# Performance work log

Measured on AMD Instinct MI355X. Metric: run time of the kernel, lower is better.

The kernel has to match this reference:

```python
import jax, jax.numpy as jnp
import numpy as np

N_NODES = 50000
N_EDGES = 500000
N_GRAPHS = 100
D = 146
N_CLASSES = 10
BN_EPS = 1e-5


def setup_inputs() -> dict:
    key = jax.random.key(0)
    ks = jax.random.split(key, 16)
    nodes_feat = jax.random.normal(ks[0], (N_NODES, D), dtype=jnp.float32)
    src = jax.random.randint(ks[1], (N_EDGES,), 0, N_NODES)
    dst = jax.random.randint(ks[2], (N_EDGES,), 0, N_NODES)
    graph_ids = jnp.sort(jax.random.randint(ks[3], (N_NODES,), 0, N_GRAPHS))
    # snorm_n = 1/sqrt(num_nodes of the graph each node belongs to)
    counts = jax.ops.segment_sum(jnp.ones((N_NODES,), jnp.float32), graph_ids, N_GRAPHS)
    counts = jnp.maximum(counts, 1.0)
    snorm_n = (1.0 / jnp.sqrt(counts))[graph_ids][:, None]
    s = 1.0 / np.sqrt(D)
    W_emb = jax.random.uniform(ks[4], (D, D), jnp.float32, -s, s)
    b_emb = jnp.zeros((D,), jnp.float32)
    # 4 stacked GCN layers (gcn_1, gcn_2, gcn_3, gcn_o)
    Ws = jax.random.uniform(ks[5], (4, D, D), jnp.float32, -s, s)
    bs = jnp.zeros((4, D), jnp.float32)
    gammas = jnp.ones((4, D), jnp.float32)
    betas = jnp.zeros((4, D), jnp.float32)
    # MLPReadout: 146 -> 73 -> 36 -> 10
    h1, h2 = D // 2, D // 4
    W_r0 = jax.random.uniform(ks[6], (D, h1), jnp.float32, -s, s)
    b_r0 = jnp.zeros((h1,), jnp.float32)
    W_r1 = jax.random.uniform(ks[7], (h1, h2), jnp.float32, -1/np.sqrt(h1), 1/np.sqrt(h1))
    b_r1 = jnp.zeros((h2,), jnp.float32)
    W_r2 = jax.random.uniform(ks[8], (h2, N_CLASSES), jnp.float32, -1/np.sqrt(h2), 1/np.sqrt(h2))
    b_r2 = jnp.zeros((N_CLASSES,), jnp.float32)
    return {"nodes_feat": nodes_feat, "snorm_n": snorm_n, "W_emb": W_emb, "b_emb": b_emb,
            "Ws": Ws, "bs": bs, "gammas": gammas, "betas": betas,
            "W_r0": W_r0, "b_r0": b_r0, "W_r1": W_r1, "b_r1": b_r1, "W_r2": W_r2, "b_r2": b_r2,
            "src": src, "dst": dst, "graph_ids": graph_ids}


def _degree_norms(src, dst):
    ones = jnp.ones((src.shape[0],), jnp.float32)
    deg_out = jnp.maximum(jax.ops.segment_sum(ones, src, N_NODES), 1.0)
    deg_in = jnp.maximum(jax.ops.segment_sum(ones, dst, N_NODES), 1.0)
    return jax.lax.rsqrt(deg_out), jax.lax.rsqrt(deg_in)


def _gcn_layer(h, W, b, gamma, beta, snorm_n, src, dst, norm_src, norm_dst):
    # DGL GraphConv(norm='both'): out = D_in^-1/2 * A^T * (D_out^-1/2 * (h W)) + b
    h_in = h
    hW = (h * norm_src[:, None]) @ W                      # [N, D]
    msg = hW[src]                                          # gather [E, D]
    agg = jax.ops.segment_sum(msg, dst, N_NODES)           # scatter-add [N, D]
    h = agg * norm_dst[:, None] + b
    h = h * snorm_n                                        # graph size norm
    # BatchNorm1d, training-mode batch statistics over nodes
    mean = jnp.mean(h, axis=0)
    var = jnp.var(h, axis=0)
    h = (h - mean) * jax.lax.rsqrt(var + BN_EPS) * gamma + beta
    h = jax.nn.relu(h)
    return h_in + h                                        # residual


def _mean_nodes(h, graph_ids):
    counts = jnp.maximum(jax.ops.segment_sum(jnp.ones((N_NODES,), h.dtype), graph_ids, N_GRAPHS), 1.0)
    return jax.ops.segment_sum(h, graph_ids, N_GRAPHS) / counts[:, None]


def reference(nodes_feat, snorm_n, W_emb, b_emb, Ws, bs, gammas, betas,
              W_r0, b_r0, W_r1, b_r1, W_r2, b_r2, src, dst, graph_ids):
    norm_src, norm_dst = _degree_norms(src, dst)
    h = nodes_feat @ W_emb + b_emb
    hg = jnp.zeros((N_GRAPHS, D), h.dtype)
    for i in range(4):
        h = _gcn_layer(h, Ws[i], bs[i], gammas[i], betas[i], snorm_n, src, dst, norm_src, norm_dst)
        hg = hg + _mean_nodes(h, graph_ids)
    # MLPReadout
    z = jax.nn.relu(hg @ W_r0 + b_r0)
    z = jax.nn.relu(z @ W_r1 + b_r1)
    return z @ W_r2 + b_r2
```

## Files before the change

### kernel.cpp

```cpp
#include <hip/hip_runtime.h>
#include <hip/hip_fp16.h>

#define D 146
#define AS 160
#define HWS 80
#define NG 100
#define BN_EPS 1e-5f

typedef _Float16 half8 __attribute__((ext_vector_type(8)));
typedef float f32x4 __attribute__((ext_vector_type(4)));

__global__ void packw_k(const float* __restrict__ Wemb, const float* __restrict__ Ws,
                        __half* __restrict__ Wf)
{
    int idx = blockIdx.x * 256 + threadIdx.x;
    if (idx >= 5 * 5 * 10 * 64 * 8) return;
    int i8 = idx & 7;
    int l  = (idx >> 3) & 63;
    int t  = (idx >> 9) % 10;
    int s  = (idx / (8 * 64 * 10)) % 5;
    int m  = idx / (8 * 64 * 10 * 5);
    int k = s * 32 + ((l >> 4) << 3) + i8;
    int c = t * 16 + (l & 15);
    float v = 0.0f;
    if (k < D && c < D) {
        const float* Wsrc = (m == 0) ? Wemb : (Ws + (size_t)(m - 1) * D * D);
        v = Wsrc[k * D + c];
    }
    Wf[idx] = __float2half(v);
}

__global__ void cvtnodes_k(const float* __restrict__ nodes, __half2* __restrict__ out2, int N)
{
    int idx = blockIdx.x * 256 + threadIdx.x;
    if (idx >= N * HWS) return;
    int r = idx / HWS, j = idx % HWS;
    int c = 2 * j;
    float v0 = (c < D) ? nodes[(size_t)r * D + c] : 0.0f;
    float v1 = (c + 1 < D) ? nodes[(size_t)r * D + c + 1] : 0.0f;
    out2[idx] = __floats2half2_rn(v0, v1);
}

__global__ void deg_k(const int* __restrict__ src, const int* __restrict__ dst,
                      int* __restrict__ co, int* __restrict__ ci, int E)
{
    int e = blockIdx.x * 256 + threadIdx.x;
    if (e >= E) return;
    atomicAdd(&co[src[e]], 1);
    atomicAdd(&ci[dst[e]], 1);
}

__global__ void rsq_k(const int* __restrict__ co, const int* __restrict__ ci,
                      float* __restrict__ ns, float* __restrict__ nd, int N)
{
    int i = blockIdx.x * 256 + threadIdx.x;
    if (i >= N) return;
    ns[i] = rsqrtf(fmaxf((float)co[i], 1.0f));
    nd[i] = rsqrtf(fmaxf((float)ci[i], 1.0f));
}

__global__ __launch_bounds__(256) void pscan1_k(const int* __restrict__ cnt,
                                                int* __restrict__ bsum, int N)
{
    __shared__ int lds[256];
    int t = blockIdx.x * 256 + threadIdx.x;
    lds[threadIdx.x] = (t < N) ? ((cnt[t] + 7) & ~7) : 0;
    __syncthreads();
    for (int s = 128; s > 0; s >>= 1) {
        if (threadIdx.x < s) lds[threadIdx.x] += lds[threadIdx.x + s];
        __syncthreads();
    }
    if (threadIdx.x == 0) bsum[blockIdx.x] = lds[0];
}

__global__ __launch_bounds__(256) void pscan2_k(const int* __restrict__ bsum,
                                                int* __restrict__ boff, int nb)
{
    __shared__ int lds[256];
    int t = threadIdx.x;
    int v = (t < nb) ? bsum[t] : 0;
    lds[t] = v;
    __syncthreads();
    for (int off = 1; off < 256; off <<= 1) {
        int u = (t >= off) ? lds[t - off] : 0;
        __syncthreads();
        lds[t] += u;
        __syncthreads();
    }
    boff[t] = lds[t] - v;
}

__global__ __launch_bounds__(256) void pscan3_k(const int* __restrict__ cnt,
                                                const int* __restrict__ boff,
                                                int* __restrict__ rowptr,
                                                int* __restrict__ cursor, int N)
{
    __shared__ int lds[256];
    int t = blockIdx.x * 256 + threadIdx.x;
    int v = (t < N) ? ((cnt[t] + 7) & ~7) : 0;
    lds[threadIdx.x] = v;
    __syncthreads();
    for (int off = 1; off < 256; off <<= 1) {
        int u = (threadIdx.x >= off) ? lds[threadIdx.x - off] : 0;
        __syncthreads();
        lds[threadIdx.x] += u;
        __syncthreads();
    }
    if (t < N) {
        int r = boff[blockIdx.x] + lds[threadIdx.x] - v;
        rowptr[t] = r;
        cursor[t] = r;
    }
    if (t == N) rowptr[N] = boff[blockIdx.x] + ((N - 1) % 256 < 255 ? 0 : 0);
}

__global__ void rowend_k(const int* __restrict__ cnt, const int* __restrict__ rowptr,
                         int* __restrict__ rowptrN, int N)
{
    if (threadIdx.x == 0 && blockIdx.x == 0)
        rowptrN[0] = rowptr[N - 1] + ((cnt[N - 1] + 7) & ~7);
}

__global__ void padfill_k(const int* __restrict__ cnt, const int* __restrict__ rowptr,
                          int* __restrict__ esrc, int N)
{
    int n = blockIdx.x * 256 + threadIdx.x;
    if (n >= N) return;
    int b = rowptr[n] + cnt[n];
    int ee = rowptr[n] + ((cnt[n] + 7) & ~7);
    for (int i = b; i < ee; ++i) esrc[i] = N;
}

__global__ void csrfill_k(const int* __restrict__ src, const int* __restrict__ dst,
                          int* __restrict__ cursor, int* __restrict__ esrc, int E)
{
    int e = blockIdx.x * 256 + threadIdx.x;
    if (e >= E) return;
    int pos = atomicAdd(&cursor[dst[e]], 1);
    esrc[pos] = src[e];
}

__global__ __launch_bounds__(256) void gemm_mfma(
    const __half* __restrict__ A16, const __half* __restrict__ Wf,
    __half* __restrict__ C16h, __half* __restrict__ H16, int nrows,
    const float* __restrict__ rowscale, const float* __restrict__ bias)
{
    int lane = threadIdx.x & 63, wave = threadIdx.x >> 6;
    int m0 = blockIdx.x * 64 + wave * 16;
    int arow = m0 + (lane & 15);
    if (arow > nrows - 1) arow = nrows - 1;
    int ak = (lane >> 4) * 8;

    f32x4 acc[10] = {};
    const half8* WfV = reinterpret_cast<const half8*>(Wf);
#pragma unroll
    for (int s = 0; s < 5; ++s) {
        half8 a = *reinterpret_cast<const half8*>(&A16[(size_t)arow * AS + s * 32 + ak]);
        const half8* wrow = WfV + (size_t)(s * 10) * 64 + lane;
#pragma unroll
        for (int t = 0; t < 10; ++t) {
            half8 b = wrow[(size_t)t * 64];
            acc[t] = __builtin_amdgcn_mfma_f32_16x16x32_f16(a, b, acc[t], 0, 0, 0);
        }
    }

    int rbase = m0 + (lane >> 4) * 4;
    int ccol = lane & 15;
    if (H16) {
        float rsv[4];
#pragma unroll
        for (int j = 0; j < 4; ++j) {
            int r = rbase + j;
            rsv[j] = (r < nrows) ? rowscale[r] : 0.0f;
        }
#pragma unroll
        for (int t = 0; t < 10; ++t) {
            int c = t * 16 + ccol;
            float bv = (c < D) ? bias[c] : 0.0f;
#pragma unroll
            for (int j = 0; j < 4; ++j) {
                int r = rbase + j;
                if (r >= nrows) continue;
                float v = acc[t][j] + bv;
                H16[(size_t)r * AS + c] = __float2half(v);
                C16h[(size_t)r * AS + c] = __float2half(v * rsv[j]);
            }
        }
    } else {
#pragma unroll
        for (int t = 0; t < 10; ++t) {
            int c = t * 16 + ccol;
            if (c >= D) continue;
#pragma unroll
            for (int j = 0; j < 4; ++j) {
                int r = rbase + j;
                if (r >= nrows) continue;
                C16h[(size_t)r * AS + c] = __float2half(acc[t][j]);
            }
        }
    }
}

__global__ __launch_bounds__(256) void agg_k(
    const __half2* __restrict__ hW2, const int* __restrict__ esrc,
    const int* __restrict__ rowptr,
    const float* __restrict__ nd, const float* __restrict__ sn,
    const float* __restrict__ bias,
    __half2* __restrict__ hpre2, float* __restrict__ stats, int N)
{
    __shared__ float rs[4][D];
    __shared__ float rq[4][D];
    int lane = threadIdx.x & 63, wave = threadIdx.x >> 6;
    int per = (N + gridDim.x - 1) / gridDim.x;
    int n0 = blockIdx.x * per;
    int n1 = min(N, n0 + per);
    int wper = (per + 3) >> 2;
    int w0 = min(n1, n0 + wave * wper);
    int w1 = min(n1, w0 + wper);

    bool v1 = lane < 9;
    int j0 = lane, j1 = 64 + lane;
    int c0 = 2 * lane, c1 = 128 + 2 * lane;
    int c1m = v1 ? c1 : 0;
    float b00 = bias[c0], b01 = bias[c0 + 1];
    float b10 = bias[c1m], b11 = bias[c1m + 1];
    float s00 = 0, s01 = 0, s10 = 0, s11 = 0, q00 = 0, q01 = 0, q10 = 0, q11 = 0;

    int e = (w0 < w1) ? rowptr[w0] : 0;
    for (int n = w0; n < w1; ++n) {
        int ee = rowptr[n + 1];
        float a00 = 0, a01 = 0, a10 = 0, a11 = 0;
        for (; e < ee; e += 8) {
            int4 i0 = *reinterpret_cast<const int4*>(&esrc[e]);
            int4 i1 = *reinterpret_cast<const int4*>(&esrc[e + 4]);
            const __half2* p0 = hW2 + (size_t)i0.x * HWS;
            const __half2* p1 = hW2 + (size_t)i0.y * HWS;
            const __half2* p2 = hW2 + (size_t)i0.z * HWS;
            const __half2* p3 = hW2 + (size_t)i0.w * HWS;
            const __half2* p4 = hW2 + (size_t)i1.x * HWS;
            const __half2* p5 = hW2 + (size_t)i1.y * HWS;
            const __half2* p6 = hW2 + (size_t)i1.z * HWS;
            const __half2* p7 = hW2 + (size_t)i1.w * HWS;
            float2 f0 = __half22float2(p0[j0]);
            float2 f1 = __half22float2(p1[j0]);
            float2 f2 = __half22float2(p2[j0]);
            float2 f3 = __half22float2(p3[j0]);
            float2 f4 = __half22float2(p4[j0]);
            float2 f5 = __half22float2(p5[j0]);
            float2 f6 = __half22float2(p6[j0]);
            float2 f7 = __half22float2(p7[j0]);
            a00 += ((f0.x + f1.x) + (f2.x + f3.x)) + ((f4.x + f5.x) + (f6.x + f7.x));
            a01 += ((f0.y + f1.y) + (f2.y + f3.y)) + ((f4.y + f5.y) + (f6.y + f7.y));
            if (v1) {
                float2 g0 = __half22float2(p0[j1]);
                float2 g1 = __half22float2(p1[j1]);
                float2 g2 = __half22float2(p2[j1]);
                float2 g3 = __half22float2(p3[j1]);
                float2 g4 = __half22float2(p4[j1]);
                float2 g5 = __half22float2(p5[j1]);
                float2 g6 = __half22float2(p6[j1]);
                float2 g7 = __half22float2(p7[j1]);
                a10 += ((g0.x + g1.x) + (g2.x + g3.x)) + ((g4.x + g5.x) + (g6.x + g7.x));
                a11 += ((g0.y + g1.y) + (g2.y + g3.y)) + ((g4.y + g5.y) + (g6.y + g7.y));
            }
        }
        float ndv = nd[n], snv = sn[n];
        float h00 = (a00 * ndv + b00) * snv;
        float h01 = (a01 * ndv + b01) * snv;
        hpre2[(size_t)n * (D / 2) + j0] = __floats2half2_rn(h00, h01);
        s00 += h00; q00 = fmaf(h00, h00, q00);
        s01 += h01; q01 = fmaf(h01, h01, q01);
        if (v1) {
            float h10 = (a10 * ndv + b10) * snv;
            float h11 = (a11 * ndv + b11) * snv;
            hpre2[(size_t)n * (D / 2) + j1] = __floats2half2_rn(h10, h11);
            s10 += h10; q10 = fmaf(h10, h10, q10);
            s11 += h11; q11 = fmaf(h11, h11, q11);
        }
    }
    rs[wave][c0] = s00; rs[wave][c0 + 1] = s01;
    rq[wave][c0] = q00; rq[wave][c0 + 1] = q01;
    if (v1) {
        rs[wave][c1] = s10; rs[wave][c1 + 1] = s11;
        rq[wave][c1] = q10; rq[wave][c1 + 1] = q11;
    }
    __syncthreads();
    for (int cc = threadIdx.x; cc < D; cc += 256) {
        atomicAdd(&stats[cc], rs[0][cc] + rs[1][cc] + rs[2][cc] + rs[3][cc]);
        atomicAdd(&stats[D + cc], rq[0][cc] + rq[1][cc] + rq[2][cc] + rq[3][cc]);
    }
}

__global__ __launch_bounds__(256) void p2hg_k(
    __half2* __restrict__ h2, const __half2* __restrict__ hpre2,
    const float* __restrict__ stats, const float* __restrict__ gamma,
    const float* __restrict__ beta, const float* __restrict__ sn,
    const float* __restrict__ nsrc, const int* __restrict__ gid,
    __half2* __restrict__ hs2, float* __restrict__ hg, int N)
{
    int lane = threadIdx.x & 63, wave = threadIdx.x >> 6;
    int per = (N + gridDim.x - 1) / gridDim.x;
    int n0 = blockIdx.x * per;
    int n1 = min(N, n0 + per);
    int wper = (per + 3) >> 2;
    int w0 = min(n1, n0 + wave * wper);
    int w1 = min(n1, w0 + wper);
    if (w0 >= w1) return;

    bool v1 = lane < 9;
    bool wr = (hs2 != nullptr);
    int j0 = lane, j1 = 64 + lane;
    int c0 = 2 * lane, c1 = 128 + 2 * lane;
    int c1m = v1 ? c1 : 0;
    float inv = 1.0f / (float)N;
    float m00 = stats[c0] * inv,     m01 = stats[c0 + 1] * inv;
    float m10 = stats[c1m] * inv,    m11 = stats[c1m + 1] * inv;
    float v00 = fmaxf(stats[D + c0] * inv - m00 * m00, 0.0f);
    float v01 = fmaxf(stats[D + c0 + 1] * inv - m01 * m01, 0.0f);
    float v10 = fmaxf(stats[D + c1m] * inv - m10 * m10, 0.0f);
    float v11 = fmaxf(stats[D + c1m + 1] * inv - m11 * m11, 0.0f);
    float r00 = rsqrtf(v00 + BN_EPS), r01 = rsqrtf(v01 + BN_EPS);
    float r10 = rsqrtf(v10 + BN_EPS), r11 = rsqrtf(v11 + BN_EPS);
    float g00 = gamma[c0], g01 = gamma[c0 + 1], t00 = beta[c0], t01 = beta[c0 + 1];
    float g10 = gamma[c1m], g11 = gamma[c1m + 1], t10 = beta[c1m], t11 = beta[c1m + 1];

    int g = gid[w0];
    float a00 = 0, a01 = 0, a10 = 0, a11 = 0;
    for (int n = w0; n < w1; ++n) {
        int gr = gid[n];
        if (gr != g) {
            atomicAdd(&hg[(size_t)g * D + c0], a00);
            atomicAdd(&hg[(size_t)g * D + c0 + 1], a01);
            if (v1) {
                atomicAdd(&hg[(size_t)g * D + c1], a10);
                atomicAdd(&hg[(size_t)g * D + c1 + 1], a11);
            }
            a00 = a01 = a10 = a11 = 0;
            g = gr;
        }
        float ns = nsrc[n];
        float w2 = sn[n]; w2 *= w2;
        float2 hv = __half22float2(h2[(size_t)n * HWS + j0]);
        float2 p0 = __half22float2(hpre2[(size_t)n * (D / 2) + j0]);
        float x0 = hv.x + fmaxf((p0.x - m00) * r00 * g00 + t00, 0.0f);
        float x1 = hv.y + fmaxf((p0.y - m01) * r01 * g01 + t01, 0.0f);
        if (wr) {
            h2[(size_t)n * HWS + j0] = __floats2half2_rn(x0, x1);
            hs2[(size_t)n * HWS + j0] = __floats2half2_rn(x0 * ns, x1 * ns);
        }
        a00 = fmaf(x0, w2, a00);
        a01 = fmaf(x1, w2, a01);
        if (v1) {
            float2 hv1 = __half22float2(h2[(size_t)n * HWS + j1]);
            float2 p1 = __half22float2(hpre2[(size_t)n * (D / 2) + j1]);
            float x2 = hv1.x + fmaxf((p1.x - m10) * r10 * g10 + t10, 0.0f);
            float x3 = hv1.y + fmaxf((p1.y - m11) * r11 * g11 + t11, 0.0f);
            if (wr) {
                h2[(size_t)n * HWS + j1] = __floats2half2_rn(x2, x3);
                hs2[(size_t)n * HWS + j1] = __floats2half2_rn(x2 * ns, x3 * ns);
            }
            a10 = fmaf(x2, w2, a10);
            a11 = fmaf(x3, w2, a11);
        }
    }
    atomicAdd(&hg[(size_t)g * D + c0], a00);
    atomicAdd(&hg[(size_t)g * D + c0 + 1], a01);
    if (v1) {
        atomicAdd(&hg[(size_t)g * D + c1], a10);
        atomicAdd(&hg[(size_t)g * D + c1 + 1], a11);
    }
}

__global__ __launch_bounds__(128) void readout_k(
    const float* __restrict__ hg,
    const float* __restrict__ W0, const float* __restrict__ b0,
    const float* __restrict__ W1, const float* __restrict__ b1,
    const float* __restrict__ W2, const float* __restrict__ b2,
    float* __restrict__ out)
{
    __shared__ float hl[D];
    __shared__ float z1[73];
    __shared__ float z2[36];
    int g = blockIdx.x;
    int t = threadIdx.x;
    for (int i = t; i < D; i += 128) hl[i] = hg[(size_t)g * D + i];
    __syncthreads();
    if (t < 73) {
        float s = b0[t];
        for (int k = 0; k < D; ++k) s = fmaf(hl[k], W0[k * 73 + t], s);
        z1[t] = fmaxf(s, 0.0f);
    }
    __syncthreads();
    if (t < 36) {
        float s = b1[t];
        for (int k = 0; k < 73; ++k) s = fmaf(z1[k], W1[k * 36 + t], s);
        z2[t] = fmaxf(s, 0.0f);
    }
    __syncthreads();
    if (t < 10) {
        float s = b2[t];
        for (int k = 0; k < 36; ++k) s = fmaf(z2[k], W2[k * 10 + t], s);
        out[g * 10 + t] = s;
    }
}

extern "C" void kernel_launch(void* const* d_in, const int* in_sizes, int n_in,
                              void* d_out, int out_size, void* d_ws, size_t ws_size,
                              hipStream_t stream)
{
    const float* nodes  = (const float*)d_in[0];
    const float* snorm  = (const float*)d_in[1];
    const float* Wemb   = (const float*)d_in[2];
    const float* bemb   = (const float*)d_in[3];
    const float* Ws     = (const float*)d_in[4];
    const float* bs     = (const float*)d_in[5];
    const float* gammas = (const float*)d_in[6];
    const float* betas  = (const float*)d_in[7];
    const float* Wr0    = (const float*)d_in[8];
    const float* br0    = (const float*)d_in[9];
    const float* Wr1    = (const float*)d_in[10];
    const float* br1    = (const float*)d_in[11];
    const float* Wr2    = (const float*)d_in[12];
    const float* br2    = (const float*)d_in[13];
    const int*   src    = (const int*)d_in[14];
    const int*   dst    = (const int*)d_in[15];
    const int*   gid    = (const int*)d_in[16];

    int N = in_sizes[0] / D;
    int E = in_sizes[14];
    int nb = (N + 255) / 256;
    const int NWF = 5 * 5 * 10 * 64 * 8;
    int Ecap = E + 8 * ((N + 7) & ~7);

    float* ws = (float*)d_ws;
    size_t off = 0;
    float* nsrc  = ws + off; off += N;
    float* ndst  = ws + off; off += N;
    float* stats = ws + off; off += 4 * 4 * D;
    float* hg    = ws + off; off += (size_t)NG * D;
    int* cnt_out = (int*)(ws + off); off += N;
    int* cnt_in  = (int*)(ws + off); off += N;
    int* rowptr  = (int*)(ws + off); off += N + 4;
    int* cursor  = (int*)(ws + off); off += N;
    int* esrc    = (int*)(ws + off); off += Ecap;
    int* bsum    = (int*)(ws + off); off += 256;
    int* boff    = (int*)(ws + off); off += 256;
    off = (off + 3) & ~(size_t)3;
    __half* Wf      = (__half*)(ws + off); off += NWF / 2;
    __half* h16     = (__half*)(ws + off); off += (size_t)N * AS / 2;
    __half* hs16    = (__half*)(ws + off); off += (size_t)N * AS / 2;
    __half* nodes16 = (__half*)(ws + off);
    __half* hW16    = (__half*)(ws + off); off += (size_t)(N + 1) * AS / 2;

    __half* hpre16  = (__half*)(ws + off); off += (size_t)N * D / 2;

    hipMemsetAsync(cnt_out, 0, 2 * (size_t)N * sizeof(int), stream);
    hipMemsetAsync(stats, 0, (16 * D + (size_t)NG * D) * sizeof(float), stream);
    hipMemsetAsync(hW16 + (size_t)N * AS, 0, AS * sizeof(__half), stream);
    packw_k<<<(NWF + 255) / 256, 256, 0, stream>>>(Wemb, Ws, Wf);
    cvtnodes_k<<<(N * HWS + 255) / 256, 256, 0, stream>>>(nodes, (__half2*)nodes16, N);
    deg_k<<<(E + 255) / 256, 256, 0, stream>>>(src, dst, cnt_out, cnt_in, E);
    rsq_k<<<(N + 255) / 256, 256, 0, stream>>>(cnt_out, cnt_in, nsrc, ndst, N);
    pscan1_k<<<nb, 256, 0, stream>>>(cnt_in, bsum, N);
    pscan2_k<<<1, 256, 0, stream>>>(bsum, boff, nb);
    pscan3_k<<<nb, 256, 0, stream>>>(cnt_in, boff, rowptr, cursor, N);
    rowend_k<<<1, 64, 0, stream>>>(cnt_in, rowptr, rowptr + N, N);
    padfill_k<<<nb, 256, 0, stream>>>(cnt_in, rowptr, esrc, N);
    csrfill_k<<<(E + 255) / 256, 256, 0, stream>>>(src, dst, cursor, esrc, E);

    int gblk = (N + 63) / 64;
    gemm_mfma<<<gblk, 256, 0, stream>>>(nodes16, Wf, hs16, h16, N, nsrc, bemb);

    for (int l = 0; l < 4; ++l) {
        float* st = stats + (size_t)l * 4 * D;
        gemm_mfma<<<gblk, 256, 0, stream>>>(hs16, Wf + (size_t)(l + 1) * (NWF / 5),
                                            hW16, nullptr, N, nullptr, nullptr);
        agg_k<<<1024, 256, 0, stream>>>((const __half2*)hW16, esrc, rowptr, ndst, snorm,
                                        bs + (size_t)l * D, (__half2*)hpre16, st, N);
        p2hg_k<<<2048, 256, 0, stream>>>((__half2*)h16, (const __half2*)hpre16, st,
                                         gammas + (size_t)l * D, betas + (size_t)l * D,
                                         snorm, nsrc, gid,
                                         (l == 3) ? nullptr : (__half2*)hs16, hg, N);
    }

    readout_k<<<NG, 128, 0, stream>>>(hg, Wr0, br0, Wr1, br1, Wr2, br2, (float*)d_out);
}
```

Baseline: 566.7 us.

## Balance aggregation work by edge count and compute two row tiles per GEMM wave

A new partition kernel binary-searches the padded CSR row pointer so that each aggregation wave gets a roughly equal share of edges instead of an equal count of nodes. The MFMA GEMM now has each wave compute two 16-row tiles that share the same weight fragments, which halves weight loads per output row. The cost is more accumulator registers per wave and half as many GEMM blocks, which could reduce occupancy and how evenly the blocks spread across compute units. A dead store of rowptr[N] in the scan kernel is also removed.

New measurement: 556.5 us. No clear change (-1.8%).

```diff
diff --git a/kernel.cpp b/kernel.cpp
--- a/kernel.cpp
+++ b/kernel.cpp
@@ -111,7 +111,6 @@
         rowptr[t] = r;
         cursor[t] = r;
     }
-    if (t == N) rowptr[N] = boff[blockIdx.x] + ((N - 1) % 256 < 255 ? 0 : 0);
 }
 
 __global__ void rowend_k(const int* __restrict__ cnt, const int* __restrict__ rowptr,
@@ -140,62 +139,120 @@
     esrc[pos] = src[e];
 }
 
+__global__ void part_k(const int* __restrict__ rowptr, int* __restrict__ wstart,
+                       int N, int NW)
+{
+    int w = blockIdx.x * 256 + threadIdx.x;
+    if (w > NW) return;
+    if (w == NW) { wstart[NW] = N; return; }
+    if (w == 0) { wstart[0] = 0; return; }
+    long long Epad = rowptr[N];
+    long long target = Epad * w / NW;
+    int lo = 0, hi = N;
+    while (lo < hi) {
+        int mid = (lo + hi) >> 1;
+        if ((long long)rowptr[mid] <= target) lo = mid + 1; else hi = mid;
+    }
+    wstart[w] = lo - 1;
+}
+
 __global__ __launch_bounds__(256) void gemm_mfma(
     const __half* __restrict__ A16, const __half* __restrict__ Wf,
     __half* __restrict__ C16h, __half* __restrict__ H16, int nrows,
     const float* __restrict__ rowscale, const float* __restrict__ bias)
 {
     int lane = threadIdx.x & 63, wave = threadIdx.x >> 6;
-    int m0 = blockIdx.x * 64 + wave * 16;
-    int arow = m0 + (lane & 15);
-    if (arow > nrows - 1) arow = nrows - 1;
+    int m0 = blockIdx.x * 128 + wave * 32;
+    int ar0 = min(m0 + (lane & 15), nrows - 1);
+    int ar1 = min(m0 + 16 + (lane & 15), nrows - 1);
     int ak = (lane >> 4) * 8;
 
-    f32x4 acc[10] = {};
+    f32x4 acc0[10] = {};
+    f32x4 acc1[10] = {};
     const half8* WfV = reinterpret_cast<const half8*>(Wf);
 #pragma unroll
     for (int s = 0; s < 5; ++s) {
-        half8 a = *reinterpret_cast<const half8*>(&A16[(size_t)arow * AS + s * 32 + ak]);
+        half8 a0 = *reinterpret_cast<const half8*>(&A16[(size_t)ar0 * AS + s * 32 + ak]);
+        half8 a1 = *reinterpret_cast<const half8*>(&A16[(size_t)ar1 * AS + s * 32 + ak]);
         const half8* wrow = WfV + (size_t)(s * 10) * 64 + lane;
 #pragma unroll
         for (int t = 0; t < 10; ++t) {
             half8 b = wrow[(size_t)t * 64];
-            acc[t] = __builtin_amdgcn_mfma_f32_16x16x32_f16(a, b, acc[t], 0, 0, 0);
-        }
-    }
-
-    int rbase = m0 + (lane >> 4) * 4;
+            acc0[t] = __builtin_amdgcn_mfma_f32_16x16x32_f16(a0, b, acc0[t], 0, 0, 0);
+            acc1[t] = __builtin_amdgcn_mfma_f32_16x16x32_f16(a1, b, acc1[t], 0, 0, 0);
+        }
+    }
+
     int ccol = lane & 15;
-    if (H16) {
-        float rsv[4];
-#pragma unroll
-        for (int j = 0; j < 4; ++j) {
-            int r = rbase + j;
-            rsv[j] = (r < nrows) ? rowscale[r] : 0.0f;
-        }
-#pragma unroll
-        for (int t = 0; t < 10; ++t) {
-            int c = t * 16 + ccol;
-            float bv = (c < D) ? bias[c] : 0.0f;
+    {
+        int rbase = m0 + (lane >> 4) * 4;
+        if (H16) {
+            float rsv[4];
 #pragma unroll
             for (int j = 0; j < 4; ++j) {
                 int r = rbase + j;
-                if (r >= nrows) continue;
-                float v = acc[t][j] + bv;
-                H16[(size_t)r * AS + c] = __float2half(v);
-                C16h[(size_t)r * AS + c] = __float2half(v * rsv[j]);
-            }
-        }
-    } else {
-#pragma unroll
-        for (int t = 0; t < 10; ++t) {
-            int c = t * 16 + ccol;
-            if (c >= D) continue;
+                rsv[j] = (r < nrows) ? rowscale[r] : 0.0f;
+            }
+#pragma unroll
+            for (int t = 0; t < 10; ++t) {
+                int c = t * 16 + ccol;
+                float bv = (c < D) ? bias[c] : 0.0f;
+#pragma unroll
+                for (int j = 0; j < 4; ++j) {
+                    int r = rbase + j;
+                    if (r >= nrows) continue;
+                    float v = acc0[t][j] + bv;
+                    H16[(size_t)r * AS + c] = __float2half(v);
+                    C16h[(size_t)r * AS + c] = __float2half(v * rsv[j]);
+                }
+            }
+        } else {
+#pragma unroll
+            for (int t = 0; t < 10; ++t) {
+                int c = t * 16 + ccol;
+                if (c >= D) continue;
+#pragma unroll
+                for (int j = 0; j < 4; ++j) {
+                    int r = rbase + j;
+                    if (r >= nrows) continue;
+                    C16h[(size_t)r * AS + c] = __float2half(acc0[t][j]);
+                }
+            }
+        }
+    }
+    {
+        int rbase = m0 + 16 + (lane >> 4) * 4;
+        if (H16) {
+            float rsv[4];
 #pragma unroll
             for (int j = 0; j < 4; ++j) {
                 int r = rbase + j;
-                if (r >= nrows) continue;
-                C16h[(size_t)r * AS + c] = __float2half(acc[t][j]);
+                rsv[j] = (r < nrows) ? rowscale[r] : 0.0f;
+            }
+#pragma unroll
+            for (int t = 0; t < 10; ++t) {
+                int c = t * 16 + ccol;
+                float bv = (c < D) ? bias[c] : 0.0f;
+#pragma unroll
+                for (int j = 0; j < 4; ++j) {
+                    int r = rbase + j;
+                    if (r >= nrows) continue;
+                    float v = acc1[t][j] + bv;
+                    H16[(size_t)r * AS + c] = __float2half(v);
+                    C16h[(size_t)r * AS + c] = __float2half(v * rsv[j]);
+                }
+            }
+        } else {
+#pragma unroll
+            for (int t = 0; t < 10; ++t) {
+                int c = t * 16 + ccol;
+                if (c >= D) continue;
+#pragma unroll
+                for (int j = 0; j < 4; ++j) {
+                    int r = rbase + j;
+                    if (r >= nrows) continue;
+                    C16h[(size_t)r * AS + c] = __float2half(acc1[t][j]);
+                }
             }
         }
     }
@@ -203,7 +260,7 @@
 
 __global__ __launch_bounds__(256) void agg_k(
     const __half2* __restrict__ hW2, const int* __restrict__ esrc,
-    const int* __restrict__ rowptr,
+    const int* __restrict__ rowptr, const int* __restrict__ wstart,
     const float* __restrict__ nd, const float* __restrict__ sn,
     const float* __restrict__ bias,
     __half2* __restrict__ hpre2, float* __restrict__ stats, int N)
@@ -211,12 +268,8 @@
     __shared__ float rs[4][D];
     __shared__ float rq[4][D];
     int lane = threadIdx.x & 63, wave = threadIdx.x >> 6;
-    int per = (N + gridDim.x - 1) / gridDim.x;
-    int n0 = blockIdx.x * per;
-    int n1 = min(N, n0 + per);
-    int wper = (per + 3) >> 2;
-    int w0 = min(n1, n0 + wave * wper);
-    int w1 = min(n1, w0 + wper);
+    int w = blockIdx.x * 4 + wave;
+    int w0 = wstart[w], w1 = wstart[w + 1];
 
     bool v1 = lane < 9;
     int j0 = lane, j1 = 64 + lane;
@@ -431,6 +484,8 @@
     int nb = (N + 255) / 256;
     const int NWF = 5 * 5 * 10 * 64 * 8;
     int Ecap = E + 8 * ((N + 7) & ~7);
+    const int AGB = 1024;
+    const int NW = AGB * 4;
 
     float* ws = (float*)d_ws;
     size_t off = 0;
@@ -445,13 +500,13 @@
     int* esrc    = (int*)(ws + off); off += Ecap;
     int* bsum    = (int*)(ws + off); off += 256;
     int* boff    = (int*)(ws + off); off += 256;
+    int* wstart  = (int*)(ws + off); off += NW + 4;
     off = (off + 3) & ~(size_t)3;
     __half* Wf      = (__half*)(ws + off); off += NWF / 2;
     __half* h16     = (__half*)(ws + off); off += (size_t)N * AS / 2;
     __half* hs16    = (__half*)(ws + off); off += (size_t)N * AS / 2;
     __half* nodes16 = (__half*)(ws + off);
     __half* hW16    = (__half*)(ws + off); off += (size_t)(N + 1) * AS / 2;
-
     __half* hpre16  = (__half*)(ws + off); off += (size_t)N * D / 2;
 
     hipMemsetAsync(cnt_out, 0, 2 * (size_t)N * sizeof(int), stream);
@@ -467,16 +522,17 @@
     rowend_k<<<1, 64, 0, stream>>>(cnt_in, rowptr, rowptr + N, N);
     padfill_k<<<nb, 256, 0, stream>>>(cnt_in, rowptr, esrc, N);
     csrfill_k<<<(E + 255) / 256, 256, 0, stream>>>(src, dst, cursor, esrc, E);
-
-    int gblk = (N + 63) / 64;
+    part_k<<<(NW + 256) / 256, 256, 0, stream>>>(rowptr, wstart, N, NW);
+
+    int gblk = (N + 127) / 128;
     gemm_mfma<<<gblk, 256, 0, stream>>>(nodes16, Wf, hs16, h16, N, nsrc, bemb);
 
     for (int l = 0; l < 4; ++l) {
         float* st = stats + (size_t)l * 4 * D;
         gemm_mfma<<<gblk, 256, 0, stream>>>(hs16, Wf + (size_t)(l + 1) * (NWF / 5),
                                             hW16, nullptr, N, nullptr, nullptr);
-        agg_k<<<1024, 256, 0, stream>>>((const __half2*)hW16, esrc, rowptr, ndst, snorm,
-                                        bs + (size_t)l * D, (__half2*)hpre16, st, N);
+        agg_k<<<AGB, 256, 0, stream>>>((const __half2*)hW16, esrc, rowptr, wstart, ndst, snorm,
+                                       bs + (size_t)l * D, (__half2*)hpre16, st, N);
         p2hg_k<<<2048, 256, 0, stream>>>((__half2*)h16, (const __half2*)hpre16, st,
                                          gammas + (size_t)l * D, betas + (size_t)l * D,
                                          snorm, nsrc, gid,
```

## Fuse CSR setup kernels, edge-balance aggregation, drop scaled-h buffer, widen GEMM tiles

Applied to the files above, without the earlier changes.

Merges rsq, rowend and padfill into pscan3 and a new finalize kernel, which also binary-searches per-wave node ranges so each aggregation wave gets an equal share of edges. The separate source-degree-scaled copy of h is removed. The GEMM now applies the row scale to its A operand in fp16, and the residual kernel no longer writes that second copy. Each GEMM wave computes 32 rows with paired half2 stores. This cuts launches and memory traffic and balances load, at the cost of rounding the scale in fp16 and higher register pressure.

Result: no change. 573.4 us (+1.2%).

```diff
diff --git a/kernel.cpp b/kernel.cpp
--- a/kernel.cpp
+++ b/kernel.cpp
@@ -50,15 +50,6 @@
     atomicAdd(&ci[dst[e]], 1);
 }
 
-__global__ void rsq_k(const int* __restrict__ co, const int* __restrict__ ci,
-                      float* __restrict__ ns, float* __restrict__ nd, int N)
-{
-    int i = blockIdx.x * 256 + threadIdx.x;
-    if (i >= N) return;
-    ns[i] = rsqrtf(fmaxf((float)co[i], 1.0f));
-    nd[i] = rsqrtf(fmaxf((float)ci[i], 1.0f));
-}
-
 __global__ __launch_bounds__(256) void pscan1_k(const int* __restrict__ cnt,
                                                 int* __restrict__ bsum, int N)
 {
@@ -93,11 +84,16 @@
 __global__ __launch_bounds__(256) void pscan3_k(const int* __restrict__ cnt,
                                                 const int* __restrict__ boff,
                                                 int* __restrict__ rowptr,
-                                                int* __restrict__ cursor, int N)
+                                                int* __restrict__ cursor,
+                                                const int* __restrict__ co,
+                                                float* __restrict__ ns,
+                                                float* __restrict__ nd, int N)
 {
     __shared__ int lds[256];
     int t = blockIdx.x * 256 + threadIdx.x;
-    int v = (t < N) ? ((cnt[t] + 7) & ~7) : 0;
+    int cv = (t < N) ? cnt[t] : 0;
+    int v = (cv + 7) & ~7;
+    if (t >= N) v = 0;
     lds[threadIdx.x] = v;
     __syncthreads();
     for (int off = 1; off < 256; off <<= 1) {
@@ -110,25 +106,9 @@
         int r = boff[blockIdx.x] + lds[threadIdx.x] - v;
         rowptr[t] = r;
         cursor[t] = r;
-    }
-    if (t == N) rowptr[N] = boff[blockIdx.x] + ((N - 1) % 256 < 255 ? 0 : 0);
-}
-
-__global__ void rowend_k(const int* __restrict__ cnt, const int* __restrict__ rowptr,
-                         int* __restrict__ rowptrN, int N)
-{
-    if (threadIdx.x == 0 && blockIdx.x == 0)
-        rowptrN[0] = rowptr[N - 1] + ((cnt[N - 1] + 7) & ~7);
-}
-
-__global__ void padfill_k(const int* __restrict__ cnt, const int* __restrict__ rowptr,
-                          int* __restrict__ esrc, int N)
-{
-    int n = blockIdx.x * 256 + threadIdx.x;
-    if (n >= N) return;
-    int b = rowptr[n] + cnt[n];
-    int ee = rowptr[n] + ((cnt[n] + 7) & ~7);
-    for (int i = b; i < ee; ++i) esrc[i] = N;
+        ns[t] = rsqrtf(fmaxf((float)co[t], 1.0f));
+        nd[t] = rsqrtf(fmaxf((float)cv, 1.0f));
+    }
 }
 
 __global__ void csrfill_k(const int* __restrict__ src, const int* __restrict__ dst,
@@ -140,62 +120,83 @@
     esrc[pos] = src[e];
 }
 
+__global__ void finalize_k(const int* __restrict__ cnt, int* __restrict__ rowptr,
+                           int* __restrict__ esrc, int* __restrict__ wstart,
+                           int N, int NW)
+{
+    int idx = blockIdx.x * 256 + threadIdx.x;
+    int Epad = rowptr[N - 1] + ((cnt[N - 1] + 7) & ~7);
+    if (idx == 0) rowptr[N] = Epad;
+    if (idx < N) {
+        int b = rowptr[idx] + cnt[idx];
+        int ee = rowptr[idx] + ((cnt[idx] + 7) & ~7);
+        for (int i = b; i < ee; ++i) esrc[i] = N;
+    }
+    if (idx <= NW) {
+        if (idx == NW) wstart[NW] = N;
+        else if (idx == 0) wstart[0] = 0;
+        else {
+            long long target = (long long)Epad * idx / NW;
+            int lo = 0, hi = N;
+            while (lo < hi) {
+                int mid = (lo + hi) >> 1;
+                if ((long long)rowptr[mid] <= target) lo = mid + 1; else hi = mid;
+            }
+            wstart[idx] = lo - 1;
+        }
+    }
+}
+
 __global__ __launch_bounds__(256) void gemm_mfma(
     const __half* __restrict__ A16, const __half* __restrict__ Wf,
-    __half* __restrict__ C16h, __half* __restrict__ H16, int nrows,
+    __half* __restrict__ OUT16, int nrows,
     const float* __restrict__ rowscale, const float* __restrict__ bias)
 {
     int lane = threadIdx.x & 63, wave = threadIdx.x >> 6;
-    int m0 = blockIdx.x * 64 + wave * 16;
-    int arow = m0 + (lane & 15);
-    if (arow > nrows - 1) arow = nrows - 1;
+    int m0 = blockIdx.x * 128 + wave * 32;
+    int ar0 = min(m0 + (lane & 15), nrows - 1);
+    int ar1 = min(m0 + 16 + (lane & 15), nrows - 1);
     int ak = (lane >> 4) * 8;
-
-    f32x4 acc[10] = {};
+    _Float16 s0 = (_Float16)(rowscale ? rowscale[ar0] : 1.0f);
+    _Float16 s1 = (_Float16)(rowscale ? rowscale[ar1] : 1.0f);
+
+    f32x4 acc0[10] = {};
+    f32x4 acc1[10] = {};
     const half8* WfV = reinterpret_cast<const half8*>(Wf);
 #pragma unroll
     for (int s = 0; s < 5; ++s) {
-        half8 a = *reinterpret_cast<const half8*>(&A16[(size_t)arow * AS + s * 32 + ak]);
+        half8 a0 = *reinterpret_cast<const half8*>(&A16[(size_t)ar0 * AS + s * 32 + ak]);
+        half8 a1 = *reinterpret_cast<const half8*>(&A16[(size_t)ar1 * AS + s * 32 + ak]);
+#pragma unroll
+        for (int i = 0; i < 8; ++i) { a0[i] *= s0; a1[i] *= s1; }
         const half8* wrow = WfV + (size_t)(s * 10) * 64 + lane;
 #pragma unroll
         for (int t = 0; t < 10; ++t) {
             half8 b = wrow[(size_t)t * 64];
-            acc[t] = __builtin_amdgcn_mfma_f32_16x16x32_f16(a, b, acc[t], 0, 0, 0);
-        }
-    }
-
-    int rbase = m0 + (lane >> 4) * 4;
+            acc0[t] = __builtin_amdgcn_mfma_f32_16x16x32_f16(a0, b, acc0[t], 0, 0, 0);
+            acc1[t] = __builtin_amdgcn_mfma_f32_16x16x32_f16(a1, b, acc1[t], 0, 0, 0);
+        }
+    }
+
     int ccol = lane & 15;
-    if (H16) {
-        float rsv[4];
-#pragma unroll
-        for (int j = 0; j < 4; ++j) {
-            int r = rbase + j;
-            rsv[j] = (r < nrows) ? rowscale[r] : 0.0f;
-        }
+    bool evenl = (lane & 1) == 0;
+    bool embed = (bias != nullptr);
+#pragma unroll
+    for (int tile = 0; tile < 2; ++tile) {
+        int rbase = m0 + tile * 16 + (lane >> 4) * 4;
+        f32x4* acc = tile ? acc1 : acc0;
 #pragma unroll
         for (int t = 0; t < 10; ++t) {
             int c = t * 16 + ccol;
-            float bv = (c < D) ? bias[c] : 0.0f;
+            float bv = (embed && c < D) ? bias[c] : 0.0f;
 #pragma unroll
             for (int j = 0; j < 4; ++j) {
                 int r = rbase + j;
-                if (r >= nrows) continue;
                 float v = acc[t][j] + bv;
-                H16[(size_t)r * AS + c] = __float2half(v);
-                C16h[(size_t)r * AS + c] = __float2half(v * rsv[j]);
-            }
-        }
-    } else {
-#pragma unroll
-        for (int t = 0; t < 10; ++t) {
-            int c = t * 16 + ccol;
-            if (c >= D) continue;
-#pragma unroll
-            for (int j = 0; j < 4; ++j) {
-                int r = rbase + j;
-                if (r >= nrows) continue;
-                C16h[(size_t)r * AS + c] = __float2half(acc[t][j]);
+                float vn = __shfl_xor(v, 1);
+                if (evenl && r < nrows && (embed || c < D))
+                    *reinterpret_cast<__half2*>(&OUT16[(size_t)r * AS + c]) =
+                        __floats2half2_rn(v, vn);
             }
         }
     }
@@ -203,7 +204,7 @@
 
 __global__ __launch_bounds__(256) void agg_k(
     const __half2* __restrict__ hW2, const int* __restrict__ esrc,
-    const int* __restrict__ rowptr,
+    const int* __restrict__ rowptr, const int* __restrict__ wstart,
     const float* __restrict__ nd, const float* __restrict__ sn,
     const float* __restrict__ bias,
     __half2* __restrict__ hpre2, float* __restrict__ stats, int N)
@@ -211,12 +212,8 @@
     __shared__ float rs[4][D];
     __shared__ float rq[4][D];
     int lane = threadIdx.x & 63, wave = threadIdx.x >> 6;
-    int per = (N + gridDim.x - 1) / gridDim.x;
-    int n0 = blockIdx.x * per;
-    int n1 = min(N, n0 + per);
-    int wper = (per + 3) >> 2;
-    int w0 = min(n1, n0 + wave * wper);
-    int w1 = min(n1, w0 + wper);
+    int w = blockIdx.x * 4 + wave;
+    int w0 = wstart[w], w1 = wstart[w + 1];
 
     bool v1 = lane < 9;
     int j0 = lane, j1 = 64 + lane;
@@ -295,8 +292,7 @@
     __half2* __restrict__ h2, const __half2* __restrict__ hpre2,
     const float* __restrict__ stats, const float* __restrict__ gamma,
     const float* __restrict__ beta, const float* __restrict__ sn,
-    const float* __restrict__ nsrc, const int* __restrict__ gid,
-    __half2* __restrict__ hs2, float* __restrict__ hg, int N)
+    const int* __restrict__ gid, float* __restrict__ hg, int N, int storeh)
 {
     int lane = threadIdx.x & 63, wave = threadIdx.x >> 6;
     int per = (N + gridDim.x - 1) / gridDim.x;
@@ -308,7 +304,6 @@
     if (w0 >= w1) return;
 
     bool v1 = lane < 9;
-    bool wr = (hs2 != nullptr);
     int j0 = lane, j1 = 64 + lane;
     int c0 = 2 * lane, c1 = 128 + 2 * lane;
     int c1m = v1 ? c1 : 0;
@@ -338,16 +333,12 @@
             a00 = a01 = a10 = a11 = 0;
             g = gr;
         }
-        float ns = nsrc[n];
         float w2 = sn[n]; w2 *= w2;
         float2 hv = __half22float2(h2[(size_t)n * HWS + j0]);
         float2 p0 = __half22float2(hpre2[(size_t)n * (D / 2) + j0]);
         float x0 = hv.x + fmaxf((p0.x - m00) * r00 * g00 + t00, 0.0f);
         float x1 = hv.y + fmaxf((p0.y - m01) * r01 * g01 + t01, 0.0f);
-        if (wr) {
-            h2[(size_t)n * HWS + j0] = __floats2half2_rn(x0, x1);
-            hs2[(size_t)n * HWS + j0] = __floats2half2_rn(x0 * ns, x1 * ns);
-        }
+        if (storeh) h2[(size_t)n * HWS + j0] = __floats2half2_rn(x0, x1);
         a00 = fmaf(x0, w2, a00);
         a01 = fmaf(x1, w2, a01);
         if (v1) {
@@ -355,10 +346,7 @@
             float2 p1 = __half22float2(hpre2[(size_t)n * (D / 2) + j1]);
             float x2 = hv1.x + fmaxf((p1.x - m10) * r10 * g10 + t10, 0.0f);
             float x3 = hv1.y + fmaxf((p1.y - m11) * r11 * g11 + t11, 0.0f);
-            if (wr) {
-                h2[(size_t)n * HWS + j1] = __floats2half2_rn(x2, x3);
-                hs2[(size_t)n * HWS + j1] = __floats2half2_rn(x2 * ns, x3 * ns);
-            }
+            if (storeh) h2[(size_t)n * HWS + j1] = __floats2half2_rn(x2, x3);
             a10 = fmaf(x2, w2, a10);
             a11 = fmaf(x3, w2, a11);
         }
@@ -431,56 +419,54 @@
     int nb = (N + 255) / 256;
     const int NWF = 5 * 5 * 10 * 64 * 8;
     int Ecap = E + 8 * ((N + 7) & ~7);
+    const int AGB = 1024;
+    const int NW = AGB * 4;
 
     float* ws = (float*)d_ws;
     size_t off = 0;
-    float* nsrc  = ws + off; off += N;
-    float* ndst  = ws + off; off += N;
     float* stats = ws + off; off += 4 * 4 * D;
     float* hg    = ws + off; off += (size_t)NG * D;
     int* cnt_out = (int*)(ws + off); off += N;
     int* cnt_in  = (int*)(ws + off); off += N;
+    size_t zbytes = (16 * D + (size_t)NG * D + 2 * (size_t)N) * 4;
+    float* nsrc  = ws + off; off += N;
+    float* ndst  = ws + off; off += N;
     int* rowptr  = (int*)(ws + off); off += N + 4;
     int* cursor  = (int*)(ws + off); off += N;
     int* esrc    = (int*)(ws + off); off += Ecap;
     int* bsum    = (int*)(ws + off); off += 256;
     int* boff    = (int*)(ws + off); off += 256;
+    int* wstart  = (int*)(ws + off); off += NW + 4;
     off = (off + 3) & ~(size_t)3;
     __half* Wf      = (__half*)(ws + off); off += NWF / 2;
     __half* h16     = (__half*)(ws + off); off += (size_t)N * AS / 2;
-    __half* hs16    = (__half*)(ws + off); off += (size_t)N * AS / 2;
     __half* nodes16 = (__half*)(ws + off);
     __half* hW16    = (__half*)(ws + off); off += (size_t)(N + 1) * AS / 2;
-
     __half* hpre16  = (__half*)(ws + off); off += (size_t)N * D / 2;
 
-    hipMemsetAsync(cnt_out, 0, 2 * (size_t)N * sizeof(int), stream);
-    hipMemsetAsync(stats, 0, (16 * D + (size_t)NG * D) * sizeof(float), stream);
+    hipMemsetAsync(stats, 0, zbytes, stream);
     hipMemsetAsync(hW16 + (size_t)N * AS, 0, AS * sizeof(__half), stream);
     packw_k<<<(NWF + 255) / 256, 256, 0, stream>>>(Wemb, Ws, Wf);
     cvtnodes_k<<<(N * HWS + 255) / 256, 256, 0, stream>>>(nodes, (__half2*)nodes16, N);
     deg_k<<<(E + 255) / 256, 256, 0, stream>>>(src, dst, cnt_out, cnt_in, E);
-    rsq_k<<<(N + 255) / 256, 256, 0, stream>>>(cnt_out, cnt_in, nsrc, ndst, N);
     pscan1_k<<<nb, 256, 0, stream>>>(cnt_in, bsum, N);
     pscan2_k<<<1, 256, 0, stream>>>(bsum, boff, nb);
-    pscan3_k<<<nb, 256, 0, stream>>>(cnt_in, boff, rowptr, cursor, N);
-    rowend_k<<<1, 64, 0, stream>>>(cnt_in, rowptr, rowptr + N, N);
-    padfill_k<<<nb, 256, 0, stream>>>(cnt_in, rowptr, esrc, N);
+    pscan3_k<<<nb, 256, 0, stream>>>(cnt_in, boff, rowptr, cursor, cnt_out, nsrc, ndst, N);
     csrfill_k<<<(E + 255) / 256, 256, 0, stream>>>(src, dst, cursor, esrc, E);
-
-    int gblk = (N + 63) / 64;
-    gemm_mfma<<<gblk, 256, 0, stream>>>(nodes16, Wf, hs16, h16, N, nsrc, bemb);
+    finalize_k<<<nb, 256, 0, stream>>>(cnt_in, rowptr, esrc, wstart, N, NW);
+
+    int gblk = (N + 127) / 128;
+    gemm_mfma<<<gblk, 256, 0, stream>>>(nodes16, Wf, h16, N, nullptr, bemb);
 
     for (int l = 0; l < 4; ++l) {
         float* st = stats + (size_t)l * 4 * D;
-        gemm_mfma<<<gblk, 256, 0, stream>>>(hs16, Wf + (size_t)(l + 1) * (NWF / 5),
-                                            hW16, nullptr, N, nullptr, nullptr);
-        agg_k<<<1024, 256, 0, stream>>>((const __half2*)hW16, esrc, rowptr, ndst, snorm,
-                                        bs + (size_t)l * D, (__half2*)hpre16, st, N);
+        gemm_mfma<<<gblk, 256, 0, stream>>>(h16, Wf + (size_t)(l + 1) * (NWF / 5),
+                                            hW16, N, nsrc, nullptr);
+        agg_k<<<AGB, 256, 0, stream>>>((const __half2*)hW16, esrc, rowptr, wstart, ndst, snorm,
+                                       bs + (size_t)l * D, (__half2*)hpre16, st, N);
         p2hg_k<<<2048, 256, 0, stream>>>((__half2*)h16, (const __half2*)hpre16, st,
                                          gammas + (size_t)l * D, betas + (size_t)l * D,
-                                         snorm, nsrc, gid,
-                                         (l == 3) ? nullptr : (__half2*)hs16, hg, N);
+                                         snorm, gid, hg, N, (l < 3) ? 1 : 0);
     }
 
     readout_k<<<NG, 128, 0, stream>>>(hg, Wr0, br0, Wr1, br1, Wr2, br2, (float*)d_out);
```
